# Kernel tuning notes

Measured on AMD Instinct MI355X. Metric: run time of the kernel, lower is better.

Reference implementation:

```python
import jax, jax.numpy as jnp
import numpy as np
from jax import lax

K = 20  # number of propagation steps (init kwarg k)


def _conv(x, w, padding):
    return lax.conv_general_dilated(
        x, w, window_strides=(1, 1), padding=padding,
        dimension_numbers=('NCHW', 'OIHW', 'NCHW'))


def _max_pool3(v):
    # 3x3 max pool, stride 1, SAME padding (pad value -inf like torch MaxPool2d)
    return lax.reduce_window(v, -jnp.inf, lax.max,
                             (1, 1, 3, 3), (1, 1, 1, 1), 'SAME')


def setup_inputs() -> dict:
    key = jax.random.key(0)
    k1, k2, k3, k4 = jax.random.split(key, 4)
    B, H, W = 16, 256, 256
    image = jax.random.uniform(k1, (B, 2, H, W), dtype=jnp.float32)
    # conv params, kaiming-ish scale
    W_h = jax.random.normal(k2, (150, 1, 3, 3), dtype=jnp.float32) * (1.0 / 3.0)
    b_h = jax.random.normal(k3, (150,), dtype=jnp.float32) * 0.1
    W_p = jax.random.normal(k4, (1, 150, 1, 1), dtype=jnp.float32) * (1.0 / np.sqrt(150.0))
    return {"image": image, "W_h": W_h, "b_h": b_h, "W_p": W_p}


def reference(image, W_h, b_h, W_p):
    occ = image[:, 0:1, :, :]  # [B,1,H,W] occupancy / free-space channel
    r = image[:, 1:2, :, :]    # [B,1,H,W] reward channel

    h = jax.nn.relu(_conv(occ, W_h, 'SAME') + b_h[None, :, None, None])  # [B,150,H,W]
    p = jax.nn.sigmoid(_conv(h, W_p, 'VALID'))                            # [B,1,H,W]

    def step(v, _):
        v = jnp.maximum(v, r + p * (_max_pool3(v) - r))
        return v, None

    v, _ = lax.scan(step, r, None, length=K)
    v = jnp.where(occ > 0.49, v, -jnp.ones_like(v))
    return v
```

## Files before the change

kernel.cpp:

```cpp
#include <hip/hip_runtime.h>
#include <hip/hip_bf16.h>
#include <math.h>


#define SENT -1e30f

typedef short short8 __attribute__((ext_vector_type(8)));
typedef float f32x16 __attribute__((ext_vector_type(16)));

__device__ __forceinline__ uint32_t pkbf(float lo, float hi) {
    uint32_t r;
    asm("v_cvt_pk_bf16_f32 %0, %1, %2" : "=v"(r) : "v"(lo), "v"(hi));
    return r;
}

__device__ __forceinline__ uint32_t bfu(float f) {
    __hip_bfloat16 h = __float2bfloat16(f);
    ushort u; __builtin_memcpy(&u, &h, 2);
    return (uint32_t)u;
}

__global__ void pack_a_kernel(const float* __restrict__ Wh,
                              const float* __restrict__ bh,
                              const float* __restrict__ Wp,
                              uint4* __restrict__ wsA)
{
    __shared__ int scan[256];
    const int tid = threadIdx.x;
    const bool valid = tid < 150;
    float wp = valid ? Wp[tid] : 0.f;
    bool pos = valid && (wp >= 0.f);
    bool neg = valid && (wp < 0.f);

    int v = (pos ? 1 : 0) | ((neg ? 1 : 0) << 16);
    scan[tid] = v;
    __syncthreads();
    for (int off = 1; off < 256; off <<= 1) {
        int x = scan[tid];
        int y = (tid >= off) ? scan[tid - off] : 0;
        __syncthreads();
        scan[tid] = x + y;
        __syncthreads();
    }
    int incl  = scan[tid];
    int total = scan[255];
    int P     = total & 0xffff;
    int rankPos = (incl & 0xffff) - (pos ? 1 : 0);
    int rankNeg = (incl >> 16)    - (neg ? 1 : 0);
    int Ppad  = (P + 31) & ~31;
    int nPosG = Ppad >> 5;
    int newidx = pos ? rankPos : (Ppad + rankNeg);

    if (tid < 384) wsA[tid] = make_uint4(0u, 0u, 0u, 0u);
    if (tid == 0)  ((uint32_t*)(wsA + 384))[0] = (uint32_t)nPosG;
    __syncthreads();

    if (valid) {
        float s  = wp;
        float w0 = Wh[tid*9+0]*s, w1 = Wh[tid*9+1]*s, w2 = Wh[tid*9+2]*s;
        float w3 = Wh[tid*9+3]*s, w4 = Wh[tid*9+4]*s, w5 = Wh[tid*9+5]*s;
        float w6 = Wh[tid*9+6]*s, w7 = Wh[tid*9+7]*s, w8 = Wh[tid*9+8]*s;
        float bb = bh[tid]*s;
        int g = newidx >> 5, col0 = newidx & 31;
        uint4 q;
        q.x = (bfu(w1) << 16) | bfu(w0);
        q.y = (bfu(w3) << 16) | bfu(w2);
        q.z = (bfu(w5) << 16) | bfu(w4);
        q.w = (bfu(w7) << 16) | bfu(w6);
        wsA[g * 64 + col0] = q;
        q.x = (bfu(bb) << 16) | bfu(w8);
        q.y = 0; q.z = 0; q.w = 0;
        wsA[g * 64 + 32 + col0] = q;
    }
}

__global__ __launch_bounds__(256, 4) void conv_p_mfma(
    const float* __restrict__ image, const uint4* __restrict__ wsA,
    float* __restrict__ pout)
{
    const int tid  = threadIdx.x;
    const int wv   = tid >> 6;
    const int lane = tid & 63;
    const int half = lane >> 5;
    const int col0 = lane & 31;
    const int b    = blockIdx.z;
    const int y    = blockIdx.y * 4 + wv;
    const int px   = blockIdx.x * 32 + col0;
    const float* occ = image + (size_t)b * 131072;

    __shared__ __align__(16) uint4 lds_a[384];
    lds_a[tid] = wsA[tid];
    if (tid < 128) lds_a[256 + tid] = wsA[256 + tid];
    uint32_t nPosG = __builtin_amdgcn_readfirstlane(((const uint32_t*)(wsA + 384))[0]);

    float t0, t1, t2, t3, t4, t5, t6, t7, t8;
    {
        bool x0ok = (px >= 1), x2ok = (px <= 254);
        int xm = px - 1, xp = px + 1;
        bool y0ok = (y >= 1), y2ok = (y <= 254);
        const float* rm = occ + (y - 1) * 256;
        const float* rc = occ + y * 256;
        const float* rp = occ + (y + 1) * 256;
        t0 = (y0ok & x0ok) ? rm[xm] : 0.f;
        t1 =  y0ok         ? rm[px] : 0.f;
        t2 = (y0ok & x2ok) ? rm[xp] : 0.f;
        t3 =  x0ok         ? rc[xm] : 0.f;
        t4 =                 rc[px];
        t5 =  x2ok         ? rc[xp] : 0.f;
        t6 = (y2ok & x0ok) ? rp[xm] : 0.f;
        t7 =  y2ok         ? rp[px] : 0.f;
        t8 = (y2ok & x2ok) ? rp[xp] : 0.f;
    }
    __syncthreads();

    union { uint32_t u[4]; short8 s; } bb;
    bb.u[0] = half ? pkbf(t8, 1.0f) : pkbf(t0, t1);
    bb.u[1] = half ? 0u : pkbf(t2, t3);
    bb.u[2] = half ? 0u : pkbf(t4, t5);
    bb.u[3] = half ? 0u : pkbf(t6, t7);
    short8 bfr = bb.s;

    const f32x16 kZero = {};
    float S0 = 0.f, S1 = 0.f, S2 = 0.f, S3 = 0.f;
#pragma unroll
    for (uint32_t g = 0; g < 6; ++g) {
        union { uint4 q; short8 s; } ua;
        ua.q = lds_a[g * 64 + lane];
        f32x16 d = __builtin_amdgcn_mfma_f32_32x32x16_bf16(ua.s, bfr, kZero, 0, 0, 0);
        if (g < nPosG) {
#pragma unroll
            for (int q = 0; q < 4; ++q) {
                S0 += fmaxf(d[q*4+0], 0.f);
                S1 += fmaxf(d[q*4+1], 0.f);
                S2 += fmaxf(d[q*4+2], 0.f);
                S3 += fmaxf(d[q*4+3], 0.f);
            }
        } else {
#pragma unroll
            for (int q = 0; q < 4; ++q) {
                S0 += fminf(d[q*4+0], 0.f);
                S1 += fminf(d[q*4+1], 0.f);
                S2 += fminf(d[q*4+2], 0.f);
                S3 += fminf(d[q*4+3], 0.f);
            }
        }
    }

    float s = (S0 + S1) + (S2 + S3);
    s += __shfl_xor(s, 32);

    float p = 1.f / (1.f + __expf(-s));
    if (!half)
        pout[(size_t)b * 65536 + y * 256 + px] = p;
}

__global__ __launch_bounds__(512, 2) void mvprop_kernel(
    const float* __restrict__ image, const float* __restrict__ pbuf,
    float* __restrict__ out)
{
    const int tid  = threadIdx.x;
    const int w    = tid >> 6;
    const int lane = tid & 63;
    const int b    = blockIdx.z;
    const int gy0  = blockIdx.y * 16 - 20;
    const int x4   = lane * 4;

    const float* rimg = image + (size_t)b * 131072 + 65536;
    const float* pp   = pbuf  + (size_t)b * 65536;

    float v[7][4], r[7][4], p[7][4];
#pragma unroll
    for (int i = 0; i < 7; ++i) {
        int gy = gy0 + w * 7 + i;
        if (gy >= 0 && gy < 256) {
            float4 rv = *(const float4*)&rimg[gy * 256 + x4];
            float4 pv = *(const float4*)&pp[gy * 256 + x4];
            r[i][0] = rv.x; r[i][1] = rv.y; r[i][2] = rv.z; r[i][3] = rv.w;
            p[i][0] = pv.x; p[i][1] = pv.y; p[i][2] = pv.z; p[i][3] = pv.w;
        } else {
            r[i][0] = r[i][1] = r[i][2] = r[i][3] = SENT;
            p[i][0] = p[i][1] = p[i][2] = p[i][3] = 0.f;
        }
        v[i][0] = r[i][0]; v[i][1] = r[i][1];
        v[i][2] = r[i][2]; v[i][3] = r[i][3];
    }

    __shared__ float4 gT[2][8][64];
    __shared__ float4 gB[2][8][64];

    for (int t = 0; t < 20; ++t) {
        int bf = t & 1;
        gT[bf][w][lane] = make_float4(v[0][0], v[0][1], v[0][2], v[0][3]);
        gB[bf][w][lane] = make_float4(v[6][0], v[6][1], v[6][2], v[6][3]);
        __syncthreads();
        float4 abv = (w > 0) ? gB[bf][w - 1][lane]
                             : make_float4(SENT, SENT, SENT, SENT);
        float4 blw = (w < 7) ? gT[bf][w + 1][lane]
                             : make_float4(SENT, SENT, SENT, SENT);

        float pv0 = abv.x, pv1 = abv.y, pv2 = abv.z, pv3 = abv.w;
#pragma unroll
        for (int i = 0; i < 7; ++i) {
            float c0 = v[i][0], c1 = v[i][1], c2 = v[i][2], c3 = v[i][3];
            float n0, n1, n2, n3;
            if (i < 6) { n0 = v[i+1][0]; n1 = v[i+1][1]; n2 = v[i+1][2]; n3 = v[i+1][3]; }
            else       { n0 = blw.x;     n1 = blw.y;     n2 = blw.z;     n3 = blw.w;     }
            float vm0 = fmaxf(pv0, fmaxf(c0, n0));
            float vm1 = fmaxf(pv1, fmaxf(c1, n1));
            float vm2 = fmaxf(pv2, fmaxf(c2, n2));
            float vm3 = fmaxf(pv3, fmaxf(c3, n3));
            float lL = __shfl_up(vm3, 1);
            lL = (lane == 0) ? SENT : lL;
            float rR = __shfl_down(vm0, 1);
            rR = (lane == 63) ? SENT : rR;
            float h0 = fmaxf(lL,  fmaxf(vm0, vm1));
            float h1 = fmaxf(vm0, fmaxf(vm1, vm2));
            float h2 = fmaxf(vm1, fmaxf(vm2, vm3));
            float h3 = fmaxf(vm2, fmaxf(vm3, rR));
            v[i][0] = fmaxf(c0, fmaf(p[i][0], h0 - r[i][0], r[i][0]));
            v[i][1] = fmaxf(c1, fmaf(p[i][1], h1 - r[i][1], r[i][1]));
            v[i][2] = fmaxf(c2, fmaf(p[i][2], h2 - r[i][2], r[i][2]));
            v[i][3] = fmaxf(c3, fmaf(p[i][3], h3 - r[i][3], r[i][3]));
            pv0 = c0; pv1 = c1; pv2 = c2; pv3 = c3;
        }
    }

    const float* occ = image + (size_t)b * 131072;
#pragma unroll
    for (int i = 0; i < 7; ++i) {
        int e = w * 7 + i;
        if (e >= 20 && e < 36) {
            int gy = gy0 + e;
            float4 ov = *(const float4*)&occ[gy * 256 + x4];
            float4 o;
            o.x = (ov.x > 0.49f) ? v[i][0] : -1.f;
            o.y = (ov.y > 0.49f) ? v[i][1] : -1.f;
            o.z = (ov.z > 0.49f) ? v[i][2] : -1.f;
            o.w = (ov.w > 0.49f) ? v[i][3] : -1.f;
            *(float4*)&out[(size_t)b * 65536 + gy * 256 + x4] = o;
        }
    }
}

extern "C" void kernel_launch(void* const* d_in, const int* in_sizes, int n_in,
                              void* d_out, int out_size, void* d_ws, size_t ws_size,
                              hipStream_t stream) {
    const float* image = (const float*)d_in[0];
    const float* Wh    = (const float*)d_in[1];
    const float* bh    = (const float*)d_in[2];
    const float* Wp    = (const float*)d_in[3];
    float* out  = (float*)d_out;
    float* pbuf = (float*)d_ws;
    uint4* wsA  = (uint4*)((char*)d_ws + (4 << 20));

    pack_a_kernel<<<1, 256, 0, stream>>>(Wh, bh, Wp, wsA);
    conv_p_mfma<<<dim3(8, 64, 16), dim3(256), 0, stream>>>(image, wsA, pbuf);
    mvprop_kernel<<<dim3(1, 16, 16), dim3(512), 0, stream>>>(image, pbuf, out);
}
```

Measured before the change: 56.00 us.

## Load MFMA weights into registers, software-pipeline epilogue, batch shuffles in propagation

```diff
diff --git a/kernel.cpp b/kernel.cpp
--- a/kernel.cpp
+++ b/kernel.cpp
@@ -18,6 +18,10 @@
     __hip_bfloat16 h = __float2bfloat16(f);
     ushort u; __builtin_memcpy(&u, &h, 2);
     return (uint32_t)u;
+}
+
+__device__ __forceinline__ float max3f(float a, float b, float c) {
+    return fmaxf(a, fmaxf(b, c));
 }
 
 __global__ void pack_a_kernel(const float* __restrict__ Wh,
@@ -74,7 +78,28 @@
     }
 }
 
-__global__ __launch_bounds__(256, 4) void conv_p_mfma(
+#define EPI(D, G)                                                            \
+    if ((G) < nPosG) {                                                       \
+        S0 += fmaxf(D[0],0.f);  S1 += fmaxf(D[1],0.f);                       \
+        S2 += fmaxf(D[2],0.f);  S3 += fmaxf(D[3],0.f);                       \
+        S0 += fmaxf(D[4],0.f);  S1 += fmaxf(D[5],0.f);                       \
+        S2 += fmaxf(D[6],0.f);  S3 += fmaxf(D[7],0.f);                       \
+        S0 += fmaxf(D[8],0.f);  S1 += fmaxf(D[9],0.f);                       \
+        S2 += fmaxf(D[10],0.f); S3 += fmaxf(D[11],0.f);                      \
+        S0 += fmaxf(D[12],0.f); S1 += fmaxf(D[13],0.f);                      \
+        S2 += fmaxf(D[14],0.f); S3 += fmaxf(D[15],0.f);                      \
+    } else {                                                                 \
+        S0 += fminf(D[0],0.f);  S1 += fminf(D[1],0.f);                       \
+        S2 += fminf(D[2],0.f);  S3 += fminf(D[3],0.f);                       \
+        S0 += fminf(D[4],0.f);  S1 += fminf(D[5],0.f);                       \
+        S2 += fminf(D[6],0.f);  S3 += fminf(D[7],0.f);                       \
+        S0 += fminf(D[8],0.f);  S1 += fminf(D[9],0.f);                       \
+        S2 += fminf(D[10],0.f); S3 += fminf(D[11],0.f);                      \
+        S0 += fminf(D[12],0.f); S1 += fminf(D[13],0.f);                      \
+        S2 += fminf(D[14],0.f); S3 += fminf(D[15],0.f);                      \
+    }
+
+__global__ __launch_bounds__(256, 5) void conv_p_mfma(
     const float* __restrict__ image, const uint4* __restrict__ wsA,
     float* __restrict__ pout)
 {
@@ -88,10 +113,10 @@
     const int px   = blockIdx.x * 32 + col0;
     const float* occ = image + (size_t)b * 131072;
 
-    __shared__ __align__(16) uint4 lds_a[384];
-    lds_a[tid] = wsA[tid];
-    if (tid < 128) lds_a[256 + tid] = wsA[256 + tid];
-    uint32_t nPosG = __builtin_amdgcn_readfirstlane(((const uint32_t*)(wsA + 384))[0]);
+    uint4 q0 = wsA[0*64+lane], q1 = wsA[1*64+lane], q2 = wsA[2*64+lane];
+    uint4 q3 = wsA[3*64+lane], q4 = wsA[4*64+lane], q5 = wsA[5*64+lane];
+    const int nPosG = (int)__builtin_amdgcn_readfirstlane(
+        ((const uint32_t*)(wsA + 384))[0]);
 
     float t0, t1, t2, t3, t4, t5, t6, t7, t8;
     {
@@ -111,7 +136,10 @@
         t7 =  y2ok         ? rp[px] : 0.f;
         t8 = (y2ok & x2ok) ? rp[xp] : 0.f;
     }
-    __syncthreads();
+
+    union UA { uint4 q; short8 s; };
+    UA u0, u1, u2, u3, u4, u5;
+    u0.q = q0; u1.q = q1; u2.q = q2; u3.q = q3; u4.q = q4; u5.q = q5;
 
     union { uint32_t u[4]; short8 s; } bb;
     bb.u[0] = half ? pkbf(t8, 1.0f) : pkbf(t0, t1);
@@ -122,29 +150,19 @@
 
     const f32x16 kZero = {};
     float S0 = 0.f, S1 = 0.f, S2 = 0.f, S3 = 0.f;
-#pragma unroll
-    for (uint32_t g = 0; g < 6; ++g) {
-        union { uint4 q; short8 s; } ua;
-        ua.q = lds_a[g * 64 + lane];
-        f32x16 d = __builtin_amdgcn_mfma_f32_32x32x16_bf16(ua.s, bfr, kZero, 0, 0, 0);
-        if (g < nPosG) {
-#pragma unroll
-            for (int q = 0; q < 4; ++q) {
-                S0 += fmaxf(d[q*4+0], 0.f);
-                S1 += fmaxf(d[q*4+1], 0.f);
-                S2 += fmaxf(d[q*4+2], 0.f);
-                S3 += fmaxf(d[q*4+3], 0.f);
-            }
-        } else {
-#pragma unroll
-            for (int q = 0; q < 4; ++q) {
-                S0 += fminf(d[q*4+0], 0.f);
-                S1 += fminf(d[q*4+1], 0.f);
-                S2 += fminf(d[q*4+2], 0.f);
-                S3 += fminf(d[q*4+3], 0.f);
-            }
-        }
-    }
+    f32x16 dc, dn;
+    dc = __builtin_amdgcn_mfma_f32_32x32x16_bf16(u0.s, bfr, kZero, 0, 0, 0);
+    dn = __builtin_amdgcn_mfma_f32_32x32x16_bf16(u1.s, bfr, kZero, 0, 0, 0);
+    EPI(dc, 0)
+    dc = __builtin_amdgcn_mfma_f32_32x32x16_bf16(u2.s, bfr, kZero, 0, 0, 0);
+    EPI(dn, 1)
+    dn = __builtin_amdgcn_mfma_f32_32x32x16_bf16(u3.s, bfr, kZero, 0, 0, 0);
+    EPI(dc, 2)
+    dc = __builtin_amdgcn_mfma_f32_32x32x16_bf16(u4.s, bfr, kZero, 0, 0, 0);
+    EPI(dn, 3)
+    dn = __builtin_amdgcn_mfma_f32_32x32x16_bf16(u5.s, bfr, kZero, 0, 0, 0);
+    EPI(dc, 4)
+    EPI(dn, 5)
 
     float s = (S0 + S1) + (S2 + S3);
     s += __shfl_xor(s, 32);
@@ -198,30 +216,42 @@
         float4 blw = (w < 7) ? gT[bf][w + 1][lane]
                              : make_float4(SENT, SENT, SENT, SENT);
 
-        float pv0 = abv.x, pv1 = abv.y, pv2 = abv.z, pv3 = abv.w;
+        float vm[7][4];
+#pragma unroll
+        for (int i = 1; i <= 5; ++i) {
+            vm[i][0] = max3f(v[i-1][0], v[i][0], v[i+1][0]);
+            vm[i][1] = max3f(v[i-1][1], v[i][1], v[i+1][1]);
+            vm[i][2] = max3f(v[i-1][2], v[i][2], v[i+1][2]);
+            vm[i][3] = max3f(v[i-1][3], v[i][3], v[i+1][3]);
+        }
+        vm[0][0] = max3f(abv.x, v[0][0], v[1][0]);
+        vm[0][1] = max3f(abv.y, v[0][1], v[1][1]);
+        vm[0][2] = max3f(abv.z, v[0][2], v[1][2]);
+        vm[0][3] = max3f(abv.w, v[0][3], v[1][3]);
+        vm[6][0] = max3f(v[5][0], v[6][0], blw.x);
+        vm[6][1] = max3f(v[5][1], v[6][1], blw.y);
+        vm[6][2] = max3f(v[5][2], v[6][2], blw.z);
+        vm[6][3] = max3f(v[5][3], v[6][3], blw.w);
+
+        float lL[7], rR[7];
 #pragma unroll
         for (int i = 0; i < 7; ++i) {
-            float c0 = v[i][0], c1 = v[i][1], c2 = v[i][2], c3 = v[i][3];
-            float n0, n1, n2, n3;
-            if (i < 6) { n0 = v[i+1][0]; n1 = v[i+1][1]; n2 = v[i+1][2]; n3 = v[i+1][3]; }
-            else       { n0 = blw.x;     n1 = blw.y;     n2 = blw.z;     n3 = blw.w;     }
-            float vm0 = fmaxf(pv0, fmaxf(c0, n0));
-            float vm1 = fmaxf(pv1, fmaxf(c1, n1));
-            float vm2 = fmaxf(pv2, fmaxf(c2, n2));
-            float vm3 = fmaxf(pv3, fmaxf(c3, n3));
-            float lL = __shfl_up(vm3, 1);
-            lL = (lane == 0) ? SENT : lL;
-            float rR = __shfl_down(vm0, 1);
-            rR = (lane == 63) ? SENT : rR;
-            float h0 = fmaxf(lL,  fmaxf(vm0, vm1));
-            float h1 = fmaxf(vm0, fmaxf(vm1, vm2));
-            float h2 = fmaxf(vm1, fmaxf(vm2, vm3));
-            float h3 = fmaxf(vm2, fmaxf(vm3, rR));
-            v[i][0] = fmaxf(c0, fmaf(p[i][0], h0 - r[i][0], r[i][0]));
-            v[i][1] = fmaxf(c1, fmaf(p[i][1], h1 - r[i][1], r[i][1]));
-            v[i][2] = fmaxf(c2, fmaf(p[i][2], h2 - r[i][2], r[i][2]));
-            v[i][3] = fmaxf(c3, fmaf(p[i][3], h3 - r[i][3], r[i][3]));
-            pv0 = c0; pv1 = c1; pv2 = c2; pv3 = c3;
+            float a = __shfl_up(vm[i][3], 1);
+            lL[i] = (lane == 0) ? SENT : a;
+            float c = __shfl_down(vm[i][0], 1);
+            rR[i] = (lane == 63) ? SENT : c;
+        }
+
+#pragma unroll
+        for (int i = 0; i < 7; ++i) {
+            float h0 = max3f(lL[i],    vm[i][0], vm[i][1]);
+            float h1 = max3f(vm[i][0], vm[i][1], vm[i][2]);
+            float h2 = max3f(vm[i][1], vm[i][2], vm[i][3]);
+            float h3 = max3f(vm[i][2], vm[i][3], rR[i]);
+            v[i][0] = fmaxf(v[i][0], fmaf(p[i][0], h0 - r[i][0], r[i][0]));
+            v[i][1] = fmaxf(v[i][1], fmaf(p[i][1], h1 - r[i][1], r[i][1]));
+            v[i][2] = fmaxf(v[i][2], fmaf(p[i][2], h2 - r[i][2], r[i][2]));
+            v[i][3] = fmaxf(v[i][3], fmaf(p[i][3], h3 - r[i][3], r[i][3]));
         }
     }
 
```

Measured after the change: 54.33 us. -3.0%, faster.
